# Optimization experiments

Hardware: AMD Instinct MI355X
Metric: run time of the kernel (lower is better)

Reference implementation:

```python
import jax, jax.numpy as jnp
import numpy as np

B, S, D = 4, 2048, 1024
H, HD = 16, 64
F = 4096
EPS = 1e-5


def layer_norm(x, gamma, beta):
    mu = jnp.mean(x, axis=-1, keepdims=True)
    var = jnp.var(x, axis=-1, keepdims=True)
    return (x - mu) * jax.lax.rsqrt(var + EPS) * gamma + beta


def setup_inputs() -> dict:
    key = jax.random.key(0)
    ks = jax.random.split(key, 16)
    s_d = 1.0 / np.sqrt(D)
    s_hd = 1.0 / np.sqrt(H * HD)
    s_f = 1.0 / np.sqrt(F)
    return {
        "x": jax.random.normal(ks[0], (B, S, D), jnp.float32),
        # per-head Q/K/V linears stacked over heads: [H, D, HD]
        "Wq": jax.random.uniform(ks[1], (H, D, HD), jnp.float32, -s_d, s_d),
        "bq": jax.random.uniform(ks[2], (H, HD), jnp.float32, -s_d, s_d),
        "Wk": jax.random.uniform(ks[3], (H, D, HD), jnp.float32, -s_d, s_d),
        "bk": jax.random.uniform(ks[4], (H, HD), jnp.float32, -s_d, s_d),
        "Wv": jax.random.uniform(ks[5], (H, D, HD), jnp.float32, -s_d, s_d),
        "bv": jax.random.uniform(ks[6], (H, HD), jnp.float32, -s_d, s_d),
        "Wo": jax.random.uniform(ks[7], (H * HD, D), jnp.float32, -s_hd, s_hd),
        "bo": jax.random.uniform(ks[8], (D,), jnp.float32, -s_hd, s_hd),
        "W1": jax.random.uniform(ks[9], (D, F), jnp.float32, -s_d, s_d),
        "b1": jax.random.uniform(ks[10], (F,), jnp.float32, -s_d, s_d),
        "W2": jax.random.uniform(ks[11], (F, D), jnp.float32, -s_f, s_f),
        "b2": jax.random.uniform(ks[12], (D,), jnp.float32, -s_f, s_f),
        "g1": jnp.ones((D,), jnp.float32),
        "be1": jnp.zeros((D,), jnp.float32),
        "g2": jnp.ones((D,), jnp.float32),
        "be2": jnp.zeros((D,), jnp.float32),
    }


def reference(x, Wq, bq, Wk, bk, Wv, bv, Wo, bo, W1, b1, W2, b2, g1, be1, g2, be2):
    scale = HD ** (-0.5)
    # per-head projections: [B,S,H,HD]
    Q = jnp.einsum("bsd,hde->bshe", x, Wq) + bq
    K = jnp.einsum("bsd,hde->bshe", x, Wk) + bk
    V = jnp.einsum("bsd,hde->bshe", x, Wv) + bv
    scores = jnp.einsum("bqhe,bkhe->bhqk", Q, K) * scale
    attn = jax.nn.softmax(scores, axis=-1)
    ctx = jnp.einsum("bhqk,bkhe->bqhe", attn, V)  # [B,S,H,HD]
    concat = ctx.reshape(B, S, H * HD)  # head-order concat
    attn_out = concat @ Wo + bo
    x1 = layer_norm(x + attn_out, g1, be1)
    ffn = jax.nn.relu(x1 @ W1 + b1) @ W2 + b2
    return layer_norm(x1 + ffn, g2, be2)
```

## Files before the change

kernel.cpp:

```cpp
#include <hip/hip_runtime.h>

#define B_ 4
#define S_ 2048
#define D_ 1024
#define H_ 16
#define HD_ 64
#define F_ 4096
#define M_ (B_*S_)
#define QS_ 3072


typedef __attribute__((ext_vector_type(8))) short bf16x8;
typedef __attribute__((ext_vector_type(4))) short short4_t;
typedef __attribute__((ext_vector_type(4))) float f32x4;
typedef __attribute__((ext_vector_type(16))) float f32x16;

#define AS1q __attribute__((address_space(1)))
#define AS3q __attribute__((address_space(3)))

__device__ __forceinline__ float bf2f(short u) {
    union { unsigned int i; float f; } v;
    v.i = ((unsigned int)(unsigned short)u) << 16;
    return v.f;
}
__device__ __forceinline__ short f2bf(float f) {
    union { float f; unsigned int i; } v; v.f = f;
    unsigned int r = v.i + 0x7fffu + ((v.i >> 16) & 1u);
    return (short)(r >> 16);
}
__device__ __forceinline__ void gld_lds16(const short* g, short* l) {
    __builtin_amdgcn_global_load_lds((const AS1q void*)g, (AS3q void*)l, 16, 0, 0);
}
__device__ __forceinline__ unsigned int cvtpk_bf16(float a, float b) {
    unsigned int r;
    asm("v_cvt_pk_bf16_f32 %0, %1, %2" : "=v"(r) : "v"(a), "v"(b));
    return r;
}
__device__ __forceinline__ float max3f(float a, float b, float c) {
    float r;
    asm("v_max3_f32 %0, %1, %2, %3" : "=v"(r) : "v"(a), "v"(b), "v"(c));
    return r;
}

__global__ __launch_bounds__(256) void cvt_f2b_k(
    const float* __restrict__ in, short* __restrict__ out, long n)
{
    long i = ((long)blockIdx.x * 256 + threadIdx.x) * 4;
    long stride = (long)gridDim.x * 256 * 4;
    for (; i < n; i += stride) {
        float4 v = *(const float4*)(in + i);
        short4_t o;
        o[0] = f2bf(v.x); o[1] = f2bf(v.y); o[2] = f2bf(v.z); o[3] = f2bf(v.w);
        *(short4_t*)(out + i) = o;
    }
}

template<typename TI>
__global__ __launch_bounds__(256) void transpose_k(
    const TI* __restrict__ in, short* __restrict__ out,
    int rows, long in_rstride,
    long in_bstrideB, long in_bstrideH, long out_bstride)
{
    __shared__ short tile[32][33];
    int z = blockIdx.z;
    const TI* ip = in + (long)(z >> 4) * in_bstrideB + (long)(z & 15) * in_bstrideH;
    short* op = out + (long)z * out_bstride;
    int r0 = blockIdx.y * 32, c0 = blockIdx.x * 32;
    int tx = threadIdx.x & 31, ty = threadIdx.x >> 5;
#pragma unroll
    for (int i = 0; i < 32; i += 8) {
        TI v = ip[(long)(r0 + ty + i) * in_rstride + (c0 + tx)];
        if constexpr (sizeof(TI) == 4) tile[ty + i][tx] = f2bf((float)v);
        else                           tile[ty + i][tx] = (short)v;
    }
    __syncthreads();
#pragma unroll
    for (int i = 0; i < 32; i += 8)
        op[(long)(c0 + ty + i) * rows + (r0 + tx)] = tile[tx][ty + i];
}

__global__ __launch_bounds__(256) void gemm_k(
    const short* __restrict__ A,
    const short* __restrict__ BT,
    const float* __restrict__ bias,
    short* __restrict__ C,
    int M, int N, int K, float scale, int relu)
{
    __shared__ short Alds[2*128*32];
    __shared__ short Blds[2*128*32];
    int tid = threadIdx.x;
    int wave = tid >> 6, lane = tid & 63;
    int lgrp = lane >> 4, lrow = lane & 15;
    int wr = wave >> 1, wc = wave & 1;
    int gx = gridDim.x;
    int nwg = gx * gridDim.y;
    int lin = blockIdx.y * gx + blockIdx.x;
    int nid = (lin & 7) * (nwg >> 3) + (lin >> 3);
    int bm = (nid / gx) * 128, bn = (nid % gx) * 128;

    int srow = wave * 32 + (lane >> 2);
    int scol = (lane & 3) * 8;
    const short* gA = A  + (long)(bm + srow) * K + scol;
    const short* gB = BT + (long)(bn + srow) * K + scol;
    short* lA0 = &Alds[(wave * 32) * 32];
    short* lA1 = &Alds[(wave * 32 + 16) * 32];
    short* lB0 = &Blds[(wave * 32) * 32];
    short* lB1 = &Blds[(wave * 32 + 16) * 32];
    long k16 = 16L * K;

    #define GSTAGE(buf, k0_) do {                              \
        gld_lds16(gA + (k0_),       lA0 + (buf)*4096);         \
        gld_lds16(gA + (k0_) + k16, lA1 + (buf)*4096);         \
        gld_lds16(gB + (k0_),       lB0 + (buf)*4096);         \
        gld_lds16(gB + (k0_) + k16, lB1 + (buf)*4096);         \
    } while (0)

    f32x4 acc[4][4] = {};
    int nk = K >> 5;
    GSTAGE(0, 0);
    __syncthreads();
    for (int t = 0; t < nk; ++t) {
        int cur = t & 1;
        if (t + 1 < nk) GSTAGE(cur ^ 1, (t + 1) * 32);
        bf16x8 af[4], bv[4];
#pragma unroll
        for (int i = 0; i < 4; i++) {
            af[i] = *(const bf16x8*)&Alds[cur*4096 + (wr*64 + i*16 + lrow) * 32 + 8*lgrp];
            bv[i] = *(const bf16x8*)&Blds[cur*4096 + (wc*64 + i*16 + lrow) * 32 + 8*lgrp];
        }
#pragma unroll
        for (int mi = 0; mi < 4; mi++)
#pragma unroll
            for (int ni = 0; ni < 4; ni++)
                acc[mi][ni] = __builtin_amdgcn_mfma_f32_16x16x32_bf16(
                    af[mi], bv[ni], acc[mi][ni], 0, 0, 0);
        __syncthreads();
    }
    #undef GSTAGE
#pragma unroll
    for (int ni = 0; ni < 4; ni++) {
        int col = bn + wc*64 + ni*16 + lrow;
        float bb = bias[col];
#pragma unroll
        for (int mi = 0; mi < 4; mi++) {
#pragma unroll
            for (int j = 0; j < 4; j++) {
                int row = bm + wr*64 + mi*16 + lgrp*4 + j;
                float v = (acc[mi][ni][j] + bb) * scale;
                if (relu) v = fmaxf(v, 0.0f);
                C[(long)row * N + col] = f2bf(v);
            }
        }
    }
}

__global__ __launch_bounds__(256) void gemm_qkv_k(
    const short* __restrict__ A,
    const short* __restrict__ BT,
    const float* __restrict__ bq,
    const float* __restrict__ bk,
    const float* __restrict__ bv,
    short* __restrict__ C,
    float qscale)
{
    __shared__ short Alds[2*128*32];
    __shared__ short Blds[2*128*32];
    const int K = 1024;
    int tid = threadIdx.x;
    int wave = tid >> 6, lane = tid & 63;
    int lgrp = lane >> 4, lrow = lane & 15;
    int wr = wave >> 1, wc = wave & 1;
    int gx = gridDim.x;
    int nwg = gx * gridDim.y;
    int lin = blockIdx.y * gx + blockIdx.x;
    int nid = (lin & 7) * (nwg >> 3) + (lin >> 3);
    int bm = (nid / gx) * 128, bn = (nid % gx) * 128;
    int seg = bn >> 10;
    const float* bp = (seg == 0) ? bq : (seg == 1) ? bk : bv;
    float scale = (seg == 0) ? qscale : 1.0f;

    int srow = wave * 32 + (lane >> 2);
    int scol = (lane & 3) * 8;
    const short* gA = A  + (long)(bm + srow) * K + scol;
    const short* gB = BT + (long)(bn + srow) * K + scol;
    short* lA0 = &Alds[(wave * 32) * 32];
    short* lA1 = &Alds[(wave * 32 + 16) * 32];
    short* lB0 = &Blds[(wave * 32) * 32];
    short* lB1 = &Blds[(wave * 32 + 16) * 32];
    long k16 = 16L * K;

    #define GSTAGE(buf, k0_) do {                              \
        gld_lds16(gA + (k0_),       lA0 + (buf)*4096);         \
        gld_lds16(gA + (k0_) + k16, lA1 + (buf)*4096);         \
        gld_lds16(gB + (k0_),       lB0 + (buf)*4096);         \
        gld_lds16(gB + (k0_) + k16, lB1 + (buf)*4096);         \
    } while (0)

    f32x4 acc[4][4] = {};
    GSTAGE(0, 0);
    __syncthreads();
    for (int t = 0; t < 32; ++t) {
        int cur = t & 1;
        if (t < 31) GSTAGE(cur ^ 1, (t + 1) * 32);
        bf16x8 af[4], bvv[4];
#pragma unroll
        for (int i = 0; i < 4; i++) {
            af[i]  = *(const bf16x8*)&Alds[cur*4096 + (wr*64 + i*16 + lrow) * 32 + 8*lgrp];
            bvv[i] = *(const bf16x8*)&Blds[cur*4096 + (wc*64 + i*16 + lrow) * 32 + 8*lgrp];
        }
#pragma unroll
        for (int mi = 0; mi < 4; mi++)
#pragma unroll
            for (int ni = 0; ni < 4; ni++)
                acc[mi][ni] = __builtin_amdgcn_mfma_f32_16x16x32_bf16(
                    af[mi], bvv[ni], acc[mi][ni], 0, 0, 0);
        __syncthreads();
    }
    #undef GSTAGE
#pragma unroll
    for (int ni = 0; ni < 4; ni++) {
        int col = bn + wc*64 + ni*16 + lrow;
        float bb = bp[col & 1023];
#pragma unroll
        for (int mi = 0; mi < 4; mi++) {
#pragma unroll
            for (int j = 0; j < 4; j++) {
                int row = bm + wr*64 + mi*16 + lgrp*4 + j;
                C[(long)row * QS_ + col] = f2bf((acc[mi][ni][j] + bb) * scale);
            }
        }
    }
}

__global__ __launch_bounds__(256) void attn_k(
    const short* __restrict__ QKV,
    const short* __restrict__ VT,
    short* __restrict__ O)
{
    __shared__ short KV[2][2][4096];
    int lin = blockIdx.y * 16 + blockIdx.x;
    int nid = (lin & 7) * 128 + (lin >> 3);
    int bh = nid >> 4, qt = nid & 15;
    int b = bh >> 4, h = bh & 15;
    int q0 = qt * 128;
    int tid = threadIdx.x, wave = tid >> 6, lane = tid & 63;
    int l31 = lane & 31, hi = lane >> 5;
    int sw = l31 & 7;

    bf16x8 aq[4];
    {
        const short* qp = QKV + (long)(b*S_ + q0 + wave*32 + l31) * QS_ + h*64 + 8*hi;
#pragma unroll
        for (int t = 0; t < 4; t++)
            aq[t] = *(const bf16x8*)(qp + 16*t);
    }
    bf16x8 ones;
#pragma unroll
    for (int i = 0; i < 8; i++) ones[i] = (short)0x3F80;

    f32x16 accO[2] = {};
    f32x16 accsum = {};
    float mj = -1e30f;

    int srow = lane >> 3;
    int schunk = (lane & 7) ^ srow;
    const short* ksrc = QKV + (long)(b*S_ + wave*16 + srow) * QS_ + 1024 + h*64 + schunk*8;
    const short* vsrc = VT + (long)bh * (64L*S_) + (long)(wave*16 + srow) * S_ + schunk*8;
    short* kd = &KV[0][0][wave*1024];
    short* vd = &KV[0][1][wave*1024];

    #define STAGE(buf, kb_) do {                                        \
        gld_lds16(ksrc + (long)(kb_)     * QS_, kd + (buf)*8192);        \
        gld_lds16(ksrc + (long)((kb_)+8) * QS_, kd + (buf)*8192 + 512);  \
        gld_lds16(vsrc + (kb_),                 vd + (buf)*8192);        \
        gld_lds16(vsrc + 8*S_ + (kb_),          vd + (buf)*8192 + 512);  \
    } while (0)

    STAGE(0, 0);
    __syncthreads();

    for (int t = 0; t < 32; ++t) {
        int cur = t & 1;
        if (t < 31) STAGE(cur ^ 1, (t + 1) * 64);
        const char* KB = (const char*)&KV[cur][0][0];
        const char* VB = (const char*)&KV[cur][1][0];

        f32x16 accs[2] = {};
#pragma unroll
        for (int c = 0; c < 2; c++) {
            bf16x8 ak[4];
#pragma unroll
            for (int tt = 0; tt < 4; tt++)
                ak[tt] = *(const bf16x8*)(KB + (32*c + l31)*128 + (((2*tt + hi) ^ sw) << 4));
            __builtin_amdgcn_s_setprio(1);
#pragma unroll
            for (int tt = 0; tt < 4; tt++)
                accs[c] = __builtin_amdgcn_mfma_f32_32x32x16_bf16(
                    ak[tt], aq[tt], accs[c], 0, 0, 0);
            __builtin_amdgcn_s_setprio(0);
        }

        float mA = fmaxf(accs[0][0], accs[0][1]);
        float mB = fmaxf(accs[1][0], accs[1][1]);
#pragma unroll
        for (int r = 2; r < 16; r += 2) {
            mA = max3f(mA, accs[0][r], accs[0][r+1]);
            mB = max3f(mB, accs[1][r], accs[1][r+1]);
        }
        float m4 = fmaxf(mA, mB);
        if (!__all(m4 <= mj + 8.0f)) {
            float m2 = fmaxf(m4, __shfl_xor(m4, 32));
            float mnew = fmaxf(mj, m2);
            float al = exp2f(mj - mnew);
            mj = mnew;
#pragma unroll
            for (int r = 0; r < 16; r++) {
                float alr = __shfl(al, (r & 3) + 8 * (r >> 2) + 4 * hi);
                accO[0][r] *= alr; accO[1][r] *= alr; accsum[r] *= alr;
            }
        }
#pragma unroll
        for (int c = 0; c < 2; c++)
#pragma unroll
            for (int r = 0; r < 16; r++)
                accs[c][r] = exp2f(accs[c][r] - mj);

        bf16x8 pa[4];
#pragma unroll
        for (int ks = 0; ks < 4; ks++) {
            int c = ks >> 1, o = (ks & 1) * 8;
            unsigned int c0 = cvtpk_bf16(accs[c][o+0], accs[c][o+1]);
            unsigned int c1 = cvtpk_bf16(accs[c][o+2], accs[c][o+3]);
            unsigned int c2 = cvtpk_bf16(accs[c][o+4], accs[c][o+5]);
            unsigned int c3 = cvtpk_bf16(accs[c][o+6], accs[c][o+7]);
            asm("v_permlane32_swap_b32 %0, %1" : "+v"(c0), "+v"(c2));
            asm("v_permlane32_swap_b32 %0, %1" : "+v"(c1), "+v"(c3));
            union { unsigned int u[4]; bf16x8 v; } pk;
            pk.u[0] = c0; pk.u[1] = c1; pk.u[2] = c2; pk.u[3] = c3;
            pa[ks] = pk.v;
        }

        __builtin_amdgcn_s_setprio(1);
#pragma unroll
        for (int eb = 0; eb < 2; eb++)
#pragma unroll
            for (int ks = 0; ks < 4; ks++) {
                bf16x8 bvf = *(const bf16x8*)(VB + (32*eb + l31)*128 + (((2*ks + hi) ^ sw) << 4));
                accO[eb] = __builtin_amdgcn_mfma_f32_32x32x16_bf16(
                    pa[ks], bvf, accO[eb], 0, 0, 0);
            }
#pragma unroll
        for (int ks = 0; ks < 4; ks++)
            accsum = __builtin_amdgcn_mfma_f32_32x32x16_bf16(
                pa[ks], ones, accsum, 0, 0, 0);
        __builtin_amdgcn_s_setprio(0);

        __syncthreads();
    }
    #undef STAGE

    const short* ob = O + (long)(b*S_) * 1024 + h*64;
#pragma unroll
    for (int r = 0; r < 16; r++) {
        int crow = (r & 3) + 8 * (r >> 2) + 4 * hi;
        float invr = 1.0f / accsum[r];
        int qr = q0 + wave*32 + crow;
#pragma unroll
        for (int eb = 0; eb < 2; eb++)
            ((short*)ob)[(long)qr * 1024 + 32*eb + l31] = f2bf(accO[eb][r] * invr);
    }
}

template<int XF32, int OUTF32>
__global__ __launch_bounds__(256) void ln_k(
    const void* __restrict__ Xv, const short* __restrict__ Y,
    const float* __restrict__ g, const float* __restrict__ be,
    void* __restrict__ Ov)
{
    int row = blockIdx.x, tid = threadIdx.x;
    long base = (long)row * 1024 + tid * 4;
    float a[4];
    if constexpr (XF32) {
        float4 xv = *(const float4*)((const float*)Xv + base);
        a[0] = xv.x; a[1] = xv.y; a[2] = xv.z; a[3] = xv.w;
    } else {
        short4_t xv = *(const short4_t*)((const short*)Xv + base);
#pragma unroll
        for (int j = 0; j < 4; j++) a[j] = bf2f(xv[j]);
    }
    short4_t yv = *(const short4_t*)(Y + base);
    float s = 0.f, s2 = 0.f;
#pragma unroll
    for (int j = 0; j < 4; j++) {
        a[j] += bf2f(yv[j]);
        s += a[j]; s2 += a[j] * a[j];
    }
#pragma unroll
    for (int off = 32; off >= 1; off >>= 1) {
        s  += __shfl_xor(s, off);
        s2 += __shfl_xor(s2, off);
    }
    __shared__ float red[8];
    if ((tid & 63) == 0) { red[(tid >> 6)*2] = s; red[(tid >> 6)*2 + 1] = s2; }
    __syncthreads();
    s  = red[0] + red[2] + red[4] + red[6];
    s2 = red[1] + red[3] + red[5] + red[7];
    float mean = s * (1.0f/1024.0f);
    float var  = s2 * (1.0f/1024.0f) - mean*mean;
    float rstd = rsqrtf(var + 1e-5f);
    float4 gv = *(const float4*)(g  + tid*4);
    float4 bv = *(const float4*)(be + tid*4);
    float r0 = (a[0] - mean) * rstd * gv.x + bv.x;
    float r1 = (a[1] - mean) * rstd * gv.y + bv.y;
    float r2 = (a[2] - mean) * rstd * gv.z + bv.z;
    float r3 = (a[3] - mean) * rstd * gv.w + bv.w;
    if constexpr (OUTF32) {
        *(float4*)((float*)Ov + base) = make_float4(r0, r1, r2, r3);
    } else {
        short4_t ov;
        ov[0] = f2bf(r0); ov[1] = f2bf(r1); ov[2] = f2bf(r2); ov[3] = f2bf(r3);
        *(short4_t*)((short*)Ov + base) = ov;
    }
}

extern "C" void kernel_launch(void* const* d_in, const int* in_sizes, int n_in,
                              void* d_out, int out_size, void* d_ws, size_t ws_size,
                              hipStream_t stream)
{
    static const int ins[17] = {0,1,2,3,4,5,6,7,8,9,10,11,12,13,14,15,16};
    static const int srt[17] = {16,4,12,2,10,5,13,3,11,0,6,1,7,14,8,15,9};
    const int* IX = (in_sizes[0] == 8388608) ? ins : srt;

    const float* x   = (const float*)d_in[IX[0]];
    const float* Wq  = (const float*)d_in[IX[1]];
    const float* bq  = (const float*)d_in[IX[2]];
    const float* Wk  = (const float*)d_in[IX[3]];
    const float* bk  = (const float*)d_in[IX[4]];
    const float* Wv  = (const float*)d_in[IX[5]];
    const float* bv  = (const float*)d_in[IX[6]];
    const float* Wo  = (const float*)d_in[IX[7]];
    const float* bo  = (const float*)d_in[IX[8]];
    const float* W1  = (const float*)d_in[IX[9]];
    const float* b1  = (const float*)d_in[IX[10]];
    const float* W2  = (const float*)d_in[IX[11]];
    const float* b2  = (const float*)d_in[IX[12]];
    const float* g1  = (const float*)d_in[IX[13]];
    const float* be1 = (const float*)d_in[IX[14]];
    const float* g2  = (const float*)d_in[IX[15]];
    const float* be2 = (const float*)d_in[IX[16]];
    short* ws  = (short*)d_ws;

    short* QKVb = ws + 0L;
    short* VTb  = ws + 25165824L;
    short* ctx  = ws + 33554432L;
    short* QKVT = ws + 41943040L;
    short* WoT  = ws + 45088768L;
    short* xb   = ws + 46137344L;
    short* W1T  = ws + 54525952L;
    short* W2T  = ws + 58720256L;
    short* x1   = ws + 0L;
    short* hb   = ws + 8388608L;
    short* ao   = ws + 46137344L;
    short* ffn  = ws + 41943040L;

    dim3 blk(256);

    cvt_f2b_k<<<2048, blk, 0, stream>>>(x, xb, (long)M_ * D_);

    transpose_k<float><<<dim3(2, 32, 16),  blk, 0, stream>>>(Wq, QKVT,            1024, 64,   0, 65536, 65536);
    transpose_k<float><<<dim3(2, 32, 16),  blk, 0, stream>>>(Wk, QKVT + 1048576L, 1024, 64,   0, 65536, 65536);
    transpose_k<float><<<dim3(2, 32, 16),  blk, 0, stream>>>(Wv, QKVT + 2097152L, 1024, 64,   0, 65536, 65536);
    transpose_k<float><<<dim3(32, 32, 1),  blk, 0, stream>>>(Wo, WoT, 1024, 1024, 0, 0, 0);
    transpose_k<float><<<dim3(128, 32, 1), blk, 0, stream>>>(W1, W1T, 1024, 4096, 0, 0, 0);
    transpose_k<float><<<dim3(32, 128, 1), blk, 0, stream>>>(W2, W2T, 4096, 1024, 0, 0, 0);

    gemm_qkv_k<<<dim3(24, 64), blk, 0, stream>>>(
        xb, QKVT, bq, bk, bv, QKVb, 0.18033688011112042f);

    transpose_k<short><<<dim3(2, 64, 64), blk, 0, stream>>>(
        QKVb + 2048, VTb, 2048, QS_, (long)S_*QS_, 64, 131072);

    attn_k<<<dim3(16, 64), blk, 0, stream>>>(QKVb, VTb, ctx);

    gemm_k<<<dim3(8, 64), blk, 0, stream>>>(ctx, WoT, bo, ao, M_, 1024, 1024, 1.0f, 0);
    ln_k<1,0><<<8192, blk, 0, stream>>>(x, ao, g1, be1, x1);

    gemm_k<<<dim3(32, 64), blk, 0, stream>>>(x1, W1T, b1, hb,  M_, 4096, 1024, 1.0f, 1);
    gemm_k<<<dim3(8, 64),  blk, 0, stream>>>(hb, W2T, b2, ffn, M_, 1024, 4096, 1.0f, 0);

    ln_k<0,1><<<8192, blk, 0, stream>>>(x1, ffn, g2, be2, d_out);
}
```

Baseline: 445.9 us.

## Fuse V transpose into QKV GEMM epilogue and lazily rescale softmax max

The QKV GEMM now writes the V segment directly in transposed per-head layout, which removes the separate transpose kernel launch and its extra read/write of V. In attention, the running negative max is preloaded into the score accumulators so the subtraction is folded into the MFMA, and the max check and rescale run only every fourth KV tile. This trades some softmax numerical headroom, since scores can drift above the current max between checks, for fewer max reductions and subtractions. The transposed V stores are 4-element short vectors, which may coalesce less well than the old transpose kernel's writes.

```diff
diff --git a/kernel.cpp b/kernel.cpp
--- a/kernel.cpp
+++ b/kernel.cpp
@@ -161,6 +161,7 @@
     const float* __restrict__ bk,
     const float* __restrict__ bv,
     short* __restrict__ C,
+    short* __restrict__ VT,
     float qscale)
 {
     __shared__ short Alds[2*128*32];
@@ -217,16 +218,35 @@
         __syncthreads();
     }
     #undef GSTAGE
-#pragma unroll
-    for (int ni = 0; ni < 4; ni++) {
-        int col = bn + wc*64 + ni*16 + lrow;
-        float bb = bp[col & 1023];
-#pragma unroll
-        for (int mi = 0; mi < 4; mi++) {
-#pragma unroll
-            for (int j = 0; j < 4; j++) {
-                int row = bm + wr*64 + mi*16 + lgrp*4 + j;
-                C[(long)row * QS_ + col] = f2bf((acc[mi][ni][j] + bb) * scale);
+    if (seg == 2) {
+        int bq0 = bm >> 11;
+#pragma unroll
+        for (int ni = 0; ni < 4; ni++) {
+            int col = bn + wc*64 + ni*16 + lrow;
+            int e   = col & 63;
+            int bh  = bq0*16 + ((col >> 6) - 32);
+            float bb = bp[col & 1023];
+#pragma unroll
+            for (int mi = 0; mi < 4; mi++) {
+                int tok = (bm + wr*64 + mi*16 + lgrp*4) & 2047;
+                short4_t o;
+#pragma unroll
+                for (int j = 0; j < 4; j++) o[j] = f2bf(acc[mi][ni][j] + bb);
+                *(short4_t*)(VT + (long)bh*131072L + (long)e*2048 + tok) = o;
+            }
+        }
+    } else {
+#pragma unroll
+        for (int ni = 0; ni < 4; ni++) {
+            int col = bn + wc*64 + ni*16 + lrow;
+            float bb = bp[col & 1023];
+#pragma unroll
+            for (int mi = 0; mi < 4; mi++) {
+#pragma unroll
+                for (int j = 0; j < 4; j++) {
+                    int row = bm + wr*64 + mi*16 + lgrp*4 + j;
+                    C[(long)row * QS_ + col] = f2bf((acc[mi][ni][j] + bb) * scale);
+                }
             }
         }
     }
@@ -260,7 +280,7 @@
 
     f32x16 accO[2] = {};
     f32x16 accsum = {};
-    float mj = -1e30f;
+    float negmj = 0.0f;
 
     int srow = lane >> 3;
     int schunk = (lane & 7) ^ srow;
@@ -285,7 +305,11 @@
         const char* KB = (const char*)&KV[cur][0][0];
         const char* VB = (const char*)&KV[cur][1][0];
 
-        f32x16 accs[2] = {};
+        f32x16 accs[2];
+#pragma unroll
+        for (int c = 0; c < 2; c++)
+#pragma unroll
+            for (int r = 0; r < 16; r++) accs[c][r] = negmj;
 #pragma unroll
         for (int c = 0; c < 2; c++) {
             bf16x8 ak[4];
@@ -300,30 +324,36 @@
             __builtin_amdgcn_s_setprio(0);
         }
 
-        float mA = fmaxf(accs[0][0], accs[0][1]);
-        float mB = fmaxf(accs[1][0], accs[1][1]);
-#pragma unroll
-        for (int r = 2; r < 16; r += 2) {
-            mA = max3f(mA, accs[0][r], accs[0][r+1]);
-            mB = max3f(mB, accs[1][r], accs[1][r+1]);
-        }
-        float m4 = fmaxf(mA, mB);
-        if (!__all(m4 <= mj + 8.0f)) {
-            float m2 = fmaxf(m4, __shfl_xor(m4, 32));
-            float mnew = fmaxf(mj, m2);
-            float al = exp2f(mj - mnew);
-            mj = mnew;
-#pragma unroll
-            for (int r = 0; r < 16; r++) {
-                float alr = __shfl(al, (r & 3) + 8 * (r >> 2) + 4 * hi);
-                accO[0][r] *= alr; accO[1][r] *= alr; accsum[r] *= alr;
+        if ((t & 3) == 0) {
+            float mA = fmaxf(accs[0][0], accs[0][1]);
+            float mB = fmaxf(accs[1][0], accs[1][1]);
+#pragma unroll
+            for (int r = 2; r < 16; r += 2) {
+                mA = max3f(mA, accs[0][r], accs[0][r+1]);
+                mB = max3f(mB, accs[1][r], accs[1][r+1]);
             }
+            float m4 = fmaxf(mA, mB);
+            if (!__all(m4 <= 8.0f)) {
+                float m2 = fmaxf(m4, __shfl_xor(m4, 32));
+                float d = fmaxf(m2, 0.0f);
+                float al = exp2f(-d);
+                negmj -= d;
+#pragma unroll
+                for (int c = 0; c < 2; c++)
+#pragma unroll
+                    for (int r = 0; r < 16; r++) accs[c][r] -= d;
+#pragma unroll
+                for (int r = 0; r < 16; r++) {
+                    float alr = __shfl(al, (r & 3) + 8 * (r >> 2) + 4 * hi);
+                    accO[0][r] *= alr; accO[1][r] *= alr; accsum[r] *= alr;
+                }
+            }
         }
 #pragma unroll
         for (int c = 0; c < 2; c++)
 #pragma unroll
             for (int r = 0; r < 16; r++)
-                accs[c][r] = exp2f(accs[c][r] - mj);
+                accs[c][r] = exp2f(accs[c][r]);
 
         bf16x8 pa[4];
 #pragma unroll
@@ -475,10 +505,7 @@
     transpose_k<float><<<dim3(32, 128, 1), blk, 0, stream>>>(W2, W2T, 4096, 1024, 0, 0, 0);
 
     gemm_qkv_k<<<dim3(24, 64), blk, 0, stream>>>(
-        xb, QKVT, bq, bk, bv, QKVb, 0.18033688011112042f);
-
-    transpose_k<short><<<dim3(2, 64, 64), blk, 0, stream>>>(
-        QKVb + 2048, VTb, 2048, QS_, (long)S_*QS_, 64, 131072);
+        xb, QKVT, bq, bk, bv, QKVb, VTb, 0.18033688011112042f);
 
     attn_k<<<dim3(16, 64), blk, 0, stream>>>(QKVb, VTb, ctx);
 
```

Measured after the change: 440.5 us. Within noise of the previous version (-1.2%).
